# Performance work log

Measured on AMD Instinct MI355X. Metric: run time of the kernel, lower is better.

The kernel has to match this reference:

```python
import math
import jax, jax.numpy as jnp
import numpy as np

LN_EPS = 1e-5
SIG_DOMAIN = 5.0


def _layer_norm(x, gamma, beta):
    mu = jnp.mean(x, axis=-1, keepdims=True)
    var = jnp.var(x, axis=-1, keepdims=True)
    return (x - mu) / jnp.sqrt(var + LN_EPS) * gamma + beta


def setup_inputs() -> dict:
    key = jax.random.key(0)
    k0, k1, k2, k3 = jax.random.split(key, 4)
    B, H, S, D = 4, 16, 1024, 256   # batch, c_heads, seq, input_dim
    A, O = 128, 256                 # attention_dim, output_dim
    x = jax.random.normal(k0, (B, H, S, D), dtype=jnp.float32)
    # torch.rand -> uniform [0,1)
    W_query = jax.random.uniform(k1, (H, A, D), dtype=jnp.float32)
    W_key = jax.random.uniform(k2, (H, A, D), dtype=jnp.float32)
    W_value = jax.random.uniform(k3, (H, O, D), dtype=jnp.float32)
    gamma = jnp.ones((D,), dtype=jnp.float32)
    beta = jnp.zeros((D,), dtype=jnp.float32)
    return {"x": x, "W_query": W_query, "W_key": W_key, "W_value": W_value,
            "gamma": gamma, "beta": beta}


def reference(x, W_query, W_key, W_value, gamma, beta):
    scale = math.sqrt(x.shape[-1])  # sqrt(input_dim)
    xn = _layer_norm(x, gamma, beta)                       # [B,H,S,D]
    q = jnp.einsum('bhsd,had->bhsa', xn, W_query)          # [B,H,S,A]
    k = jnp.einsum('bhsd,had->bhsa', xn, W_key)            # [B,H,S,A]
    v = jnp.einsum('bhsd,hod->bhso', xn, W_value)          # [B,H,S,O]
    scores = jnp.einsum('bhsa,bhta->bhst', q, k) / scale   # [B,H,S,S]
    # overtaking-sigmoid-tuned normalization
    s_max = jnp.max(scores, axis=-1, keepdims=True)
    s_min = jnp.min(scores, axis=-1, keepdims=True)
    s_norm = (scores - s_min) / (s_max - s_min)
    softmax_sel = 1.0 - jax.nn.sigmoid(
        (1.0 - jnp.max(s_norm, axis=-1, keepdims=True)) * 2.0 * SIG_DOMAIN + SIG_DOMAIN)
    sigmoid_sel = 1.0 - softmax_sel
    weights = (softmax_sel * jax.nn.softmax(s_norm, axis=-1)
               + sigmoid_sel * jax.nn.sigmoid(s_norm * 2.0 * SIG_DOMAIN - SIG_DOMAIN))
    return jnp.einsum('bhst,bhto->bhso', weights, v)       # [B,H,S,O]
```

## Files before the change

kernel.cpp:

```cpp
#include <hip/hip_runtime.h>

typedef __attribute__((ext_vector_type(8))) short bf16x8;
typedef __attribute__((ext_vector_type(8))) _Float16 h16x8;
typedef __attribute__((ext_vector_type(2))) _Float16 h16x2;
typedef __attribute__((ext_vector_type(2))) __fp16 fp16x2;
typedef __attribute__((ext_vector_type(4))) float f32x4;
typedef __attribute__((ext_vector_type(4))) unsigned short us4;
typedef unsigned short u16;

#define MFMA16  __builtin_amdgcn_mfma_f32_16x16x32_bf16
#define MFMA16H __builtin_amdgcn_mfma_f32_16x16x32_f16

__device__ __forceinline__ u16 f2bf(float f) {
  union { float f; unsigned u; } v; v.f = f;
  unsigned r = v.u + 0x7FFFu + ((v.u >> 16) & 1u);
  return (u16)(r >> 16);
}

__device__ __forceinline__ float ex2(float x) {
#if __has_builtin(__builtin_amdgcn_exp2f)
  return __builtin_amdgcn_exp2f(x);
#else
  return exp2f(x);
#endif
}

__device__ __forceinline__ h16x8 sigmoid8(h16x8 sv, float am, float bm) {
  h16x8 pa;
  h16x2* pw = (h16x2*)&pa;
  #pragma unroll
  for (int q = 0; q < 4; q++) {
    float e0 = ex2(fmaf((float)sv[2*q],     am, bm));
    float e1 = ex2(fmaf((float)sv[2*q + 1], am, bm));
    fp16x2 pk = __builtin_amdgcn_cvt_pkrtz(__builtin_amdgcn_rcpf(1.0f + e0),
                                           __builtin_amdgcn_rcpf(1.0f + e1));
    pw[q] = __builtin_bit_cast(h16x2, pk);
  }
  return pa;
}

__global__ __launch_bounds__(256) void ln_kernel(const float* __restrict__ x,
    const float* __restrict__ gamma, const float* __restrict__ beta,
    u16* __restrict__ xn)
{
  int row = blockIdx.x * 4 + (threadIdx.x >> 6);
  int lane = threadIdx.x & 63;
  const float* xr = x + (size_t)row * 256;
  f32x4 v = *(const f32x4*)(xr + lane * 4);
  float s  = v[0] + v[1] + v[2] + v[3];
  float s2 = v[0]*v[0] + v[1]*v[1] + v[2]*v[2] + v[3]*v[3];
  #pragma unroll
  for (int off = 1; off < 64; off <<= 1) {
    s  += __shfl_xor(s, off);
    s2 += __shfl_xor(s2, off);
  }
  float mu   = s * (1.0f / 256.0f);
  float var  = s2 * (1.0f / 256.0f) - mu * mu;
  float rstd = rsqrtf(var + 1e-5f);
  f32x4 g  = *(const f32x4*)(gamma + lane * 4);
  f32x4 bb = *(const f32x4*)(beta  + lane * 4);
  us4 o;
  #pragma unroll
  for (int j = 0; j < 4; j++) o[j] = f2bf((v[j] - mu) * rstd * g[j] + bb[j]);
  *(us4*)(xn + (size_t)row * 256 + lane * 4) = o;
}

__global__ __launch_bounds__(256) void cvt_kernel(const float* __restrict__ in,
    u16* __restrict__ out, int n4)
{
  int i = blockIdx.x * 256 + threadIdx.x;
  if (i >= n4) return;
  f32x4 v = *(const f32x4*)(in + (size_t)i * 4);
  us4 o;
  #pragma unroll
  for (int j = 0; j < 4; j++) o[j] = f2bf(v[j]);
  *(us4*)(out + (size_t)i * 4) = o;
}

__global__ __launch_bounds__(256) void cvt_qk(const float* __restrict__ in,
    u16* __restrict__ out, int half)
{
  int i = blockIdx.x * 256 + threadIdx.x;
  int e4 = i * 4;
  int h = e4 >> 15;
  int rem = e4 & 32767;
  f32x4 v = *(const f32x4*)(in + e4);
  us4 o;
  #pragma unroll
  for (int j = 0; j < 4; j++) o[j] = f2bf(v[j]);
  *(us4*)(out + (size_t)h * 65536 + half * 32768 + rem) = o;
}

__global__ __launch_bounds__(256) void gemm128(const u16* __restrict__ Ag,
    const u16* __restrict__ Bg, u16* __restrict__ Cg,
    int M, int N, int aHead, int bHead, int outHalf)
{
  constexpr int K = 256;
  __shared__ u16 As[128][128];
  __shared__ u16 Bs[128][128];
  int bh = blockIdx.z;
  int m0 = blockIdx.x * 128, n0 = blockIdx.y * 128;
  const u16* Ab = Ag + (size_t)(aHead ? (bh & 15) : bh) * M * K + (size_t)m0 * K;
  const u16* Bb = Bg + (size_t)(bHead ? (bh & 15) : bh) * N * K + (size_t)n0 * K;
  int tid = threadIdx.x, lane = tid & 63, w = tid >> 6;
  int wm = w >> 1, wn = w & 1;
  int lr = lane & 15, g = lane >> 4;

  f32x4 acc[4][4] = {};
  for (int kc = 0; kc < 2; kc++) {
    if (kc) __syncthreads();
    #pragma unroll
    for (int i = 0; i < 8; i++) {
      int c = tid + 256 * i;
      int r = c >> 4, ch = c & 15;
      int sw = (ch ^ (r & 7)) * 8;
      *(bf16x8*)&As[r][sw] = *(const bf16x8*)(Ab + (size_t)r * K + kc * 128 + ch * 8);
      *(bf16x8*)&Bs[r][sw] = *(const bf16x8*)(Bb + (size_t)r * K + kc * 128 + ch * 8);
    }
    __syncthreads();
    #pragma unroll
    for (int ks = 0; ks < 4; ks++) {
      bf16x8 af[4], bfr[4];
      #pragma unroll
      for (int mf = 0; mf < 4; mf++) {
        int r = wm * 64 + mf * 16 + lr;
        af[mf] = *(const bf16x8*)&As[r][((ks * 4 + g) ^ (r & 7)) * 8];
      }
      #pragma unroll
      for (int nf = 0; nf < 4; nf++) {
        int r = wn * 64 + nf * 16 + lr;
        bfr[nf] = *(const bf16x8*)&Bs[r][((ks * 4 + g) ^ (r & 7)) * 8];
      }
      #pragma unroll
      for (int mf = 0; mf < 4; mf++)
        #pragma unroll
        for (int nf = 0; nf < 4; nf++)
          acc[mf][nf] = MFMA16(af[mf], bfr[nf], acc[mf][nf], 0, 0, 0);
    }
  }
  u16* Cb = Cg + (size_t)bh * M * N;
  #pragma unroll
  for (int mf = 0; mf < 4; mf++)
    #pragma unroll
    for (int nf = 0; nf < 4; nf++)
      #pragma unroll
      for (int i = 0; i < 4; i++) {
        int row = m0 + wm * 64 + mf * 16 + g * 4 + i;
        int col = n0 + wn * 64 + nf * 16 + lr;
        u16 ev;
        if (outHalf) { _Float16 hv = (_Float16)acc[mf][nf][i]; ev = *(u16*)&hv; }
        else ev = f2bf(acc[mf][nf][i]);
        Cb[(size_t)row * N + col] = ev;
      }
}

__global__ __launch_bounds__(256) void score_kernel(
    const u16* __restrict__ QKg, _Float16* __restrict__ Sg, float2* __restrict__ rp, int bh0)
{
  constexpr int S = 1024, LD = 256;
  __shared__ u16 Qs[128][128];
  __shared__ u16 Ks[128][128];
  int bid = blockIdx.x;
  int hl = ((bid >> 6) << 3) | (bid & 7);
  int rb = (bid >> 3) & 7;
  int bh = bh0 + hl;
  int m0 = rb * 128;
  int tid = threadIdx.x, lane = tid & 63, w = tid >> 6;
  int lr = lane & 15, g = lane >> 4;
  const u16* Qb = QKg + ((size_t)bh * S + m0) * LD;
  const u16* Kb = QKg + (size_t)bh * S * LD + 128;

  #pragma unroll
  for (int i = 0; i < 8; i++) {
    int c = tid + 256 * i;
    int r = c >> 4, ch = c & 15;
    *(bf16x8*)&Qs[r][(ch ^ (r & 7)) * 8] = *(const bf16x8*)(Qb + (size_t)r * LD + ch * 8);
    *(bf16x8*)&Ks[r][(ch ^ (r & 7)) * 8] = *(const bf16x8*)(Kb + (size_t)r * LD + ch * 8);
  }
  __syncthreads();

  bf16x8 aq[2][4];
  #pragma unroll
  for (int mf = 0; mf < 2; mf++)
    #pragma unroll
    for (int ks = 0; ks < 4; ks++) {
      int r = w * 32 + mf * 16 + lr;
      aq[mf][ks] = *(const bf16x8*)&Qs[r][((ks * 4 + g) ^ (r & 7)) * 8];
    }

  float rmin[2][4], rmax[2][4];
  #pragma unroll
  for (int mf = 0; mf < 2; mf++)
    #pragma unroll
    for (int i = 0; i < 4; i++) { rmin[mf][i] = 3.0e38f; rmax[mf][i] = -3.0e38f; }

  _Float16* Sb = Sg + (size_t)hl * S * S;
  for (int nc = 0; nc < 8; nc++) {
    bf16x8 kreg[8];
    if (nc < 7) {
      #pragma unroll
      for (int i = 0; i < 8; i++) {
        int c = tid + 256 * i;
        int r = c >> 4, ch = c & 15;
        kreg[i] = *(const bf16x8*)(Kb + (size_t)(128 * (nc + 1) + r) * LD + ch * 8);
      }
    }
    f32x4 acc[2][8] = {};
    #pragma unroll
    for (int ks = 0; ks < 4; ks++) {
      bf16x8 bk[8];
      #pragma unroll
      for (int nf = 0; nf < 8; nf++) {
        int r = nf * 16 + lr;
        bk[nf] = *(const bf16x8*)&Ks[r][((ks * 4 + g) ^ (r & 7)) * 8];
      }
      #pragma unroll
      for (int mf = 0; mf < 2; mf++)
        #pragma unroll
        for (int nf = 0; nf < 8; nf++)
          acc[mf][nf] = MFMA16(aq[mf][ks], bk[nf], acc[mf][nf], 0, 0, 0);
    }
    #pragma unroll
    for (int mf = 0; mf < 2; mf++)
      #pragma unroll
      for (int nf = 0; nf < 8; nf++)
        #pragma unroll
        for (int i = 0; i < 4; i++) {
          int row = m0 + w * 32 + mf * 16 + g * 4 + i;
          int col = nc * 128 + nf * 16 + lr;
          Sb[(size_t)row * S + col] = (_Float16)acc[mf][nf][i];
          rmin[mf][i] = fminf(rmin[mf][i], acc[mf][nf][i]);
          rmax[mf][i] = fmaxf(rmax[mf][i], acc[mf][nf][i]);
        }
    __syncthreads();
    if (nc < 7) {
      #pragma unroll
      for (int i = 0; i < 8; i++) {
        int c = tid + 256 * i;
        int r = c >> 4, ch = c & 15;
        *(bf16x8*)&Ks[r][(ch ^ (r & 7)) * 8] = kreg[i];
      }
    }
    __syncthreads();
  }
  #pragma unroll
  for (int off = 1; off < 16; off <<= 1)
    #pragma unroll
    for (int mf = 0; mf < 2; mf++)
      #pragma unroll
      for (int i = 0; i < 4; i++) {
        rmin[mf][i] = fminf(rmin[mf][i], __shfl_xor(rmin[mf][i], off));
        rmax[mf][i] = fmaxf(rmax[mf][i], __shfl_xor(rmax[mf][i], off));
      }
  if (lr == 0) {
    #pragma unroll
    for (int mf = 0; mf < 2; mf++)
      #pragma unroll
      for (int i = 0; i < 4; i++) {
        int row = m0 + w * 32 + mf * 16 + g * 4 + i;
        float inv = 1.0f / (rmax[mf][i] - rmin[mf][i]);
        rp[(size_t)bh * S + row] = make_float2(10.0f * inv, fmaf(-10.0f * rmin[mf][i], inv, -5.0f));
      }
  }
}

__global__ __launch_bounds__(256, 4) void pv_kernel(
    const _Float16* __restrict__ Sg, const float2* __restrict__ rpG,
    const u16* __restrict__ VTg, float* __restrict__ Out, int bh0)
{
  constexpr int S = 1024, OD = 256;
  __shared__ char Bs[2][256 * 64];
  int bid = blockIdx.x;
  int hl = ((bid >> 7) << 3) | (bid & 7);
  int rb = (bid >> 3) & 15;
  int bh = bh0 + hl;
  int m0 = rb * 64;
  int tid = threadIdx.x, lane = tid & 63, w = tid >> 6;
  int lr = lane & 15, g = lane >> 4;
  const _Float16* Sb = Sg + (size_t)hl * S * S;
  const u16* Vb = VTg + (size_t)bh * OD * S;

  int qrow = m0 + w * 16 + lr;
  float2 pp = rpG[(size_t)bh * S + qrow];
  float am = -pp.x * 1.44269504f, bm = -pp.y * 1.44269504f;
  const _Float16* Srow = Sb + (size_t)qrow * S + g * 8;

  const u16* Vg = Vb + (size_t)tid * S;
  char* wr0 = &Bs[0][tid * 64];
  char* wr1 = &Bs[1][tid * 64];
  int wsw = (tid & 3) << 4;
  int rsw = (lr & 3) << 4;

  f32x4 acc[16] = {};

  h16x8 sv0 = *(const h16x8*)(Srow);
  h16x8 sv1 = *(const h16x8*)(Srow + 32);
  h16x8 sv2 = *(const h16x8*)(Srow + 64);
  bf16x8 pre[4];
  #pragma unroll
  for (int i = 0; i < 4; i++) pre[i] = *(const bf16x8*)(Vg + i * 8);
  #pragma unroll
  for (int i = 0; i < 4; i++) *(bf16x8*)(wr0 + ((i * 16) ^ wsw)) = pre[i];
  __syncthreads();

  for (int kt = 0; kt < 32; kt++) {
    int cur = kt & 1;
    if (kt < 31) {
      #pragma unroll
      for (int i = 0; i < 4; i++)
        pre[i] = *(const bf16x8*)(Vg + (kt + 1) * 32 + i * 8);
    }
    h16x8 svn;
    if (kt < 29) svn = *(const h16x8*)(Srow + (size_t)(kt + 3) * 32);
    h16x8 pa = sigmoid8(sv0, am, bm);
    __builtin_amdgcn_s_setprio(1);
    #pragma unroll
    for (int nf = 0; nf < 16; nf++) {
      h16x8 bv = *(const h16x8*)&Bs[cur][(nf * 16 + lr) * 64 + ((g * 16) ^ rsw)];
      acc[nf] = MFMA16H(pa, bv, acc[nf], 0, 0, 0);
    }
    __builtin_amdgcn_s_setprio(0);
    if (kt < 31) {
      char* wr = cur ? wr0 : wr1;
      #pragma unroll
      for (int i = 0; i < 4; i++) *(bf16x8*)(wr + ((i * 16) ^ wsw)) = pre[i];
    }
    sv0 = sv1; sv1 = sv2; sv2 = svn;
    __syncthreads();
  }

  const float c2 = 0.9933071490757153f;
  float* Ob = Out + ((size_t)bh * S + m0 + w * 16) * OD;
  #pragma unroll
  for (int nf = 0; nf < 16; nf++)
    #pragma unroll
    for (int i = 0; i < 4; i++)
      Ob[(size_t)(g * 4 + i) * OD + nf * 16 + lr] = c2 * acc[nf][i];
}

extern "C" void kernel_launch(void* const* d_in, const int* in_sizes, int n_in,
                              void* d_out, int out_size, void* d_ws, size_t ws_size,
                              hipStream_t stream) {
  const float* x     = (const float*)d_in[0];
  const float* Wq    = (const float*)d_in[1];
  const float* Wk    = (const float*)d_in[2];
  const float* Wv    = (const float*)d_in[3];
  const float* gamma = (const float*)d_in[4];
  const float* beta  = (const float*)d_in[5];
  float* out = (float*)d_out;

  constexpr int B = 4, H = 16, S = 1024, D = 256, A = 128, O = 256;
  constexpr int BH = B * H;

  char* p = (char*)d_ws;
  size_t off = 0;
  auto take = [&](size_t n) { off = (off + 255) & ~(size_t)255; char* q = p + off; off += n; return q; };

  u16*    xn   = (u16*)take((size_t)BH * S * D * 2);
  u16*    qkb  = (u16*)take((size_t)BH * S * 256 * 2);
  u16*    vtb  = (u16*)take((size_t)BH * O * S * 2);
  u16*    wqkb = (u16*)take((size_t)H * 256 * D * 2);
  u16*    wvb  = (u16*)take((size_t)H * O * D * 2);
  float2* rp   = (float2*)take((size_t)BH * S * 8);

  int grp = 1;
  for (; grp < 8; grp <<= 1) {
    size_t need = ((off + 255) & ~(size_t)255) + (size_t)(BH / grp) * S * S * 2;
    if (need <= ws_size) break;
  }
  int hp = BH / grp;
  _Float16* sG = (_Float16*)take((size_t)hp * S * S * 2);

  ln_kernel<<<BH * S / 4, 256, 0, stream>>>(x, gamma, beta, xn);

  cvt_qk<<<(H * A * D / 4) / 256, 256, 0, stream>>>(Wq, wqkb, 0);
  cvt_qk<<<(H * A * D / 4) / 256, 256, 0, stream>>>(Wk, wqkb, 1);
  cvt_kernel<<<(H * O * D / 4 + 255) / 256, 256, 0, stream>>>(Wv, wvb, H * O * D / 4);

  gemm128<<<dim3(S / 128, 256 / 128, BH), 256, 0, stream>>>(xn, wqkb, qkb, S, 256, 0, 1, 0);
  gemm128<<<dim3(O / 128, S / 128, BH), 256, 0, stream>>>(wvb, xn, vtb, O, S, 1, 0, 1);

  for (int gi = 0; gi < grp; gi++) {
    int bh0 = gi * hp;
    score_kernel<<<hp * 8, 256, 0, stream>>>(qkb, sG, rp, bh0);
    pv_kernel<<<hp * 16, 256, 0, stream>>>(sG, rp, vtb, out, bh0);
  }
}
```

Before: 208.3 us.

## Recompute QK scores inside PV kernel instead of materializing fp16 score matrix

```diff
diff --git a/kernel.cpp b/kernel.cpp
--- a/kernel.cpp
+++ b/kernel.cpp
@@ -2,7 +2,6 @@
 
 typedef __attribute__((ext_vector_type(8))) short bf16x8;
 typedef __attribute__((ext_vector_type(8))) _Float16 h16x8;
-typedef __attribute__((ext_vector_type(2))) _Float16 h16x2;
 typedef __attribute__((ext_vector_type(2))) __fp16 fp16x2;
 typedef __attribute__((ext_vector_type(4))) float f32x4;
 typedef __attribute__((ext_vector_type(4))) unsigned short us4;
@@ -23,20 +22,6 @@
 #else
   return exp2f(x);
 #endif
-}
-
-__device__ __forceinline__ h16x8 sigmoid8(h16x8 sv, float am, float bm) {
-  h16x8 pa;
-  h16x2* pw = (h16x2*)&pa;
-  #pragma unroll
-  for (int q = 0; q < 4; q++) {
-    float e0 = ex2(fmaf((float)sv[2*q],     am, bm));
-    float e1 = ex2(fmaf((float)sv[2*q + 1], am, bm));
-    fp16x2 pk = __builtin_amdgcn_cvt_pkrtz(__builtin_amdgcn_rcpf(1.0f + e0),
-                                           __builtin_amdgcn_rcpf(1.0f + e1));
-    pw[q] = __builtin_bit_cast(h16x2, pk);
-  }
-  return pa;
 }
 
 __global__ __launch_bounds__(256) void ln_kernel(const float* __restrict__ x,
@@ -154,16 +139,15 @@
       }
 }
 
-__global__ __launch_bounds__(256) void score_kernel(
-    const u16* __restrict__ QKg, _Float16* __restrict__ Sg, float2* __restrict__ rp, int bh0)
+__global__ __launch_bounds__(256) void minmax_kernel(
+    const u16* __restrict__ QKg, float2* __restrict__ rp)
 {
   constexpr int S = 1024, LD = 256;
   __shared__ u16 Qs[128][128];
   __shared__ u16 Ks[128][128];
   int bid = blockIdx.x;
-  int hl = ((bid >> 6) << 3) | (bid & 7);
+  int bh = ((bid >> 6) << 3) | (bid & 7);
   int rb = (bid >> 3) & 7;
-  int bh = bh0 + hl;
   int m0 = rb * 128;
   int tid = threadIdx.x, lane = tid & 63, w = tid >> 6;
   int lr = lane & 15, g = lane >> 4;
@@ -194,7 +178,6 @@
     #pragma unroll
     for (int i = 0; i < 4; i++) { rmin[mf][i] = 3.0e38f; rmax[mf][i] = -3.0e38f; }
 
-  _Float16* Sb = Sg + (size_t)hl * S * S;
   for (int nc = 0; nc < 8; nc++) {
     bf16x8 kreg[8];
     if (nc < 7) {
@@ -226,9 +209,6 @@
       for (int nf = 0; nf < 8; nf++)
         #pragma unroll
         for (int i = 0; i < 4; i++) {
-          int row = m0 + w * 32 + mf * 16 + g * 4 + i;
-          int col = nc * 128 + nf * 16 + lr;
-          Sb[(size_t)row * S + col] = (_Float16)acc[mf][nf][i];
           rmin[mf][i] = fminf(rmin[mf][i], acc[mf][nf][i]);
           rmax[mf][i] = fmaxf(rmax[mf][i], acc[mf][nf][i]);
         }
@@ -264,43 +244,39 @@
   }
 }
 
-__global__ __launch_bounds__(256, 4) void pv_kernel(
-    const _Float16* __restrict__ Sg, const float2* __restrict__ rpG,
-    const u16* __restrict__ VTg, float* __restrict__ Out, int bh0)
-{
-  constexpr int S = 1024, OD = 256;
-  __shared__ char Bs[2][256 * 64];
+__global__ __launch_bounds__(256) void attn_pv(
+    const u16* __restrict__ QKg, const float2* __restrict__ rpG,
+    const u16* __restrict__ VTg, float* __restrict__ Out)
+{
+  constexpr int S = 1024, LD = 256, OD = 256, VSTR = 40, PSTR = 40;
+  __shared__ u16 V_lds[2][256 * VSTR];
+  __shared__ u16 P_lds[4][16][PSTR];
   int bid = blockIdx.x;
-  int hl = ((bid >> 7) << 3) | (bid & 7);
+  int bh = ((bid >> 7) << 3) | (bid & 7);
   int rb = (bid >> 3) & 15;
-  int bh = bh0 + hl;
-  int m0 = rb * 64;
   int tid = threadIdx.x, lane = tid & 63, w = tid >> 6;
   int lr = lane & 15, g = lane >> 4;
-  const _Float16* Sb = Sg + (size_t)hl * S * S;
-  const u16* Vb = VTg + (size_t)bh * OD * S;
-
-  int qrow = m0 + w * 16 + lr;
-  float2 pp = rpG[(size_t)bh * S + qrow];
+  int qb = rb * 64 + w * 16;
+
+  const u16* Qb = QKg + (size_t)bh * S * LD;
+  const u16* Kb = Qb + 128;
+  const u16* Vg = VTg + ((size_t)bh * OD + tid) * S;
+
+  bf16x8 bq[4];
+  #pragma unroll
+  for (int ks = 0; ks < 4; ks++)
+    bq[ks] = *(const bf16x8*)(Qb + (size_t)(qb + lr) * LD + ks * 32 + g * 8);
+
+  float2 pp = rpG[(size_t)bh * S + qb + lr];
   float am = -pp.x * 1.44269504f, bm = -pp.y * 1.44269504f;
-  const _Float16* Srow = Sb + (size_t)qrow * S + g * 8;
-
-  const u16* Vg = Vb + (size_t)tid * S;
-  char* wr0 = &Bs[0][tid * 64];
-  char* wr1 = &Bs[1][tid * 64];
-  int wsw = (tid & 3) << 4;
-  int rsw = (lr & 3) << 4;
 
   f32x4 acc[16] = {};
 
-  h16x8 sv0 = *(const h16x8*)(Srow);
-  h16x8 sv1 = *(const h16x8*)(Srow + 32);
-  h16x8 sv2 = *(const h16x8*)(Srow + 64);
   bf16x8 pre[4];
   #pragma unroll
   for (int i = 0; i < 4; i++) pre[i] = *(const bf16x8*)(Vg + i * 8);
   #pragma unroll
-  for (int i = 0; i < 4; i++) *(bf16x8*)(wr0 + ((i * 16) ^ wsw)) = pre[i];
+  for (int i = 0; i < 4; i++) *(bf16x8*)&V_lds[0][tid * VSTR + i * 8] = pre[i];
   __syncthreads();
 
   for (int kt = 0; kt < 32; kt++) {
@@ -310,32 +286,50 @@
       for (int i = 0; i < 4; i++)
         pre[i] = *(const bf16x8*)(Vg + (kt + 1) * 32 + i * 8);
     }
-    h16x8 svn;
-    if (kt < 29) svn = *(const h16x8*)(Srow + (size_t)(kt + 3) * 32);
-    h16x8 pa = sigmoid8(sv0, am, bm);
+    #pragma unroll
+    for (int st = 0; st < 2; st++) {
+      int t0 = kt * 32 + st * 16;
+      f32x4 s = {0.f, 0.f, 0.f, 0.f};
+      #pragma unroll
+      for (int ks = 0; ks < 4; ks++) {
+        bf16x8 ak = *(const bf16x8*)(Kb + (size_t)(t0 + lr) * LD + ks * 32 + g * 8);
+        s = MFMA16(ak, bq[ks], s, 0, 0, 0);
+      }
+      float p0 = __builtin_amdgcn_rcpf(1.0f + ex2(fmaf(s[0], am, bm)));
+      float p1 = __builtin_amdgcn_rcpf(1.0f + ex2(fmaf(s[1], am, bm)));
+      float p2 = __builtin_amdgcn_rcpf(1.0f + ex2(fmaf(s[2], am, bm)));
+      float p3 = __builtin_amdgcn_rcpf(1.0f + ex2(fmaf(s[3], am, bm)));
+      fp16x2 pkA = __builtin_amdgcn_cvt_pkrtz(p0, p1);
+      fp16x2 pkB = __builtin_amdgcn_cvt_pkrtz(p2, p3);
+      uint2 pk;
+      pk.x = __builtin_bit_cast(unsigned, pkA);
+      pk.y = __builtin_bit_cast(unsigned, pkB);
+      *(uint2*)&P_lds[w][lr][st * 16 + g * 4] = pk;
+    }
+    h16x8 pb = *(const h16x8*)&P_lds[w][lr][g * 8];
     __builtin_amdgcn_s_setprio(1);
     #pragma unroll
-    for (int nf = 0; nf < 16; nf++) {
-      h16x8 bv = *(const h16x8*)&Bs[cur][(nf * 16 + lr) * 64 + ((g * 16) ^ rsw)];
-      acc[nf] = MFMA16H(pa, bv, acc[nf], 0, 0, 0);
+    for (int of = 0; of < 16; of++) {
+      h16x8 va = *(const h16x8*)&V_lds[cur][(of * 16 + lr) * VSTR + g * 8];
+      acc[of] = MFMA16H(va, pb, acc[of], 0, 0, 0);
     }
     __builtin_amdgcn_s_setprio(0);
     if (kt < 31) {
-      char* wr = cur ? wr0 : wr1;
-      #pragma unroll
-      for (int i = 0; i < 4; i++) *(bf16x8*)(wr + ((i * 16) ^ wsw)) = pre[i];
-    }
-    sv0 = sv1; sv1 = sv2; sv2 = svn;
+      #pragma unroll
+      for (int i = 0; i < 4; i++) *(bf16x8*)&V_lds[cur ^ 1][tid * VSTR + i * 8] = pre[i];
+    }
     __syncthreads();
   }
 
   const float c2 = 0.9933071490757153f;
-  float* Ob = Out + ((size_t)bh * S + m0 + w * 16) * OD;
-  #pragma unroll
-  for (int nf = 0; nf < 16; nf++)
-    #pragma unroll
-    for (int i = 0; i < 4; i++)
-      Ob[(size_t)(g * 4 + i) * OD + nf * 16 + lr] = c2 * acc[nf][i];
+  float* Ob = Out + ((size_t)bh * S + qb + lr) * OD;
+  #pragma unroll
+  for (int of = 0; of < 16; of++) {
+    f32x4 v = acc[of];
+    #pragma unroll
+    for (int i = 0; i < 4; i++) v[i] *= c2;
+    *(f32x4*)(Ob + of * 16 + g * 4) = v;
+  }
 }
 
 extern "C" void kernel_launch(void* const* d_in, const int* in_sizes, int n_in,
@@ -363,14 +357,6 @@
   u16*    wvb  = (u16*)take((size_t)H * O * D * 2);
   float2* rp   = (float2*)take((size_t)BH * S * 8);
 
-  int grp = 1;
-  for (; grp < 8; grp <<= 1) {
-    size_t need = ((off + 255) & ~(size_t)255) + (size_t)(BH / grp) * S * S * 2;
-    if (need <= ws_size) break;
-  }
-  int hp = BH / grp;
-  _Float16* sG = (_Float16*)take((size_t)hp * S * S * 2);
-
   ln_kernel<<<BH * S / 4, 256, 0, stream>>>(x, gamma, beta, xn);
 
   cvt_qk<<<(H * A * D / 4) / 256, 256, 0, stream>>>(Wq, wqkb, 0);
@@ -380,9 +366,6 @@
   gemm128<<<dim3(S / 128, 256 / 128, BH), 256, 0, stream>>>(xn, wqkb, qkb, S, 256, 0, 1, 0);
   gemm128<<<dim3(O / 128, S / 128, BH), 256, 0, stream>>>(wvb, xn, vtb, O, S, 1, 0, 1);
 
-  for (int gi = 0; gi < grp; gi++) {
-    int bh0 = gi * hp;
-    score_kernel<<<hp * 8, 256, 0, stream>>>(qkb, sG, rp, bh0);
-    pv_kernel<<<hp * 16, 256, 0, stream>>>(sG, rp, vtb, out, bh0);
-  }
-}
+  minmax_kernel<<<BH * 8, 256, 0, stream>>>(qkb, rp);
+  attn_pv<<<BH * 16, 256, 0, stream>>>(qkb, rp, vtb, out);
+}
```

After: 278.6 us. 33.8% more time.
